# Optimization experiments

Measured on AMD Instinct MI355X. Metric: run time of the kernel, lower is better.

## Reference

```python
import jax, jax.numpy as jnp
import numpy as np

T, B, I, H, K = 200, 2048, 128, 128, 4


def setup_inputs() -> dict:
    key = jax.random.key(0)
    ks = jax.random.split(key, 7)
    inputs = jax.random.normal(ks[0], (T, B, I), jnp.float32)
    lengths = jax.random.randint(ks[1], (B,), 1, T + 1, jnp.int32)
    si = 1.0 / np.sqrt(I)
    sh = 1.0 / np.sqrt(H)
    w0 = jax.random.uniform(ks[2], (H,), jnp.float32, -sh, sh)      # Linear(H,1,bias=False)
    w1_w = jax.random.uniform(ks[3], (H, I), jnp.float32, -si, si)  # Linear(I,H)
    w1_b = jax.random.uniform(ks[4], (H,), jnp.float32, -si, si)
    w2_w = jax.random.uniform(ks[5], (H, I), jnp.float32, -si, si)  # Linear(I,H,bias=False)
    w3_w = jax.random.uniform(ks[6], (H, I), jnp.float32, -si, si)  # Linear(I,H,bias=False)
    return dict(inputs=inputs, lengths=lengths, label_len=4,
                w0=w0, w1_w=w1_w, w1_b=w1_b, w2_w=w2_w, w3_w=w3_w)


def reference(inputs, lengths, label_len, w0, w1_w, w1_b, w2_w, w3_w):
    # inputs: [T, B, I] time-major padded sequences; lengths: [B]
    T_, B_, _ = inputs.shape
    Kl = label_len
    dt = inputs.dtype
    # packed semantics: padded positions are exactly zero
    valid = (jnp.arange(T_)[:, None] < lengths[None, :])  # [T, B]
    x = inputs * valid[..., None].astype(dt)
    x1 = x @ w1_w.T + w1_b                                 # [T, B, H]
    x2 = x @ w2_w.T                                        # [T, B, H]
    # running mean m_s[t] = mean(inputs[:t+1]) (zeros at padding, as in torch)
    m_s = jnp.cumsum(x, axis=0) / jnp.arange(1, T_ + 1, dtype=dt)[:, None, None]
    # labeled timesteps: last min(L, label_len) steps of each sequence
    start = jnp.maximum(lengths - Kl, 0)                   # [B]
    t_lab = start[:, None] + jnp.arange(Kl)[None, :]       # [B, K]
    lab_valid = t_lab < lengths[:, None]                   # [B, K]
    t_c = jnp.minimum(t_lab, T_ - 1)
    b_idx = jnp.arange(B_)[:, None]
    x2_lab = x2[t_c, b_idx]                                # [B, K, H]
    wms_lab = m_s[t_c, b_idx] @ w3_w.T                     # [B, K, H]
    c = x2_lab + wms_lab                                   # [B, K, H]
    # att[b,k,s] = w0 . sigmoid(x1[s,b] + x2[t_k,b] + wms[t_k,b])
    att = jnp.einsum('sbkh,h->bks',
                     jax.nn.sigmoid(x1[:, :, None, :] + c[None, :, :, :]), w0)
    causal = (jnp.arange(T_)[None, None, :] <= t_lab[:, :, None]) & lab_valid[:, :, None]
    att = att * causal.astype(dt)                          # [B, K, T]
    h = jnp.einsum('bks,sbh->bkh', att, x1) + x2_lab       # [B, K, H]
    return h * lab_valid[..., None].astype(dt)
```

## Files before the change

kernel.cpp:

```cpp
#include <hip/hip_runtime.h>
#include <stdint.h>

#define T_DIM 200
#define B_DIM 2048
#define I_DIM 128
#define H_DIM 128
#define TS    32

typedef float  f32x4  __attribute__((ext_vector_type(4)));
typedef __bf16 bf16x8 __attribute__((ext_vector_type(8)));

union BF8 { ushort4 u2[2]; bf16x8 v; };

static __device__ __forceinline__ unsigned short f2bf(float f) {
    union { __bf16 b; unsigned short u; } c; c.b = (__bf16)f; return c.u;
}
static __device__ __forceinline__ float bf2f(unsigned short s) {
    union { unsigned u; float f; } c; c.u = ((unsigned)s) << 16;
    return c.f;
}
static __device__ __forceinline__ ushort4 cvt4(float4 v) {
    return make_ushort4(f2bf(v.x), f2bf(v.y), f2bf(v.z), f2bf(v.w));
}

__global__ __launch_bounds__(256, 4) void fused_kernel(
    const float* __restrict__ x, const int* __restrict__ lengths,
    const float* __restrict__ w0, const float* __restrict__ w1,
    const float* __restrict__ b1, const float* __restrict__ w2,
    const float* __restrict__ w3, float* __restrict__ out)
{
    __shared__ __align__(16) unsigned short xs[TS][136];
    __shared__ __align__(16) unsigned short x1s[TS][130];
    __shared__ __align__(16) float attp[TS][36];
    __shared__ __align__(16) float attk[TS][4];
    __shared__ __align__(16) float ektL[H_DIM][4];
    __shared__ __align__(16) float x2ls[4][H_DIM];
    __shared__ __align__(16) float w0s[H_DIM];
    __shared__ __align__(16) unsigned short axl[4][136];
    __shared__ __align__(16) unsigned short ams[4][136];

    const int b    = blockIdx.x;
    const int tid  = threadIdx.x;
    const int lane = tid & 63;
    const int wv   = tid >> 6;
    const int l15  = lane & 15;
    const int quad = lane >> 4;
    const int L     = lengths[b];
    const int start = (L > 4) ? (L - 4) : 0;
    const int nv    = (L < 4) ? L : 4;

    if (tid < 128) w0s[tid] = w0[tid];

    const int i = tid & 127;
    const float* xp = x + (size_t)b * I_DIM + i;
    float v0 = 0.f, v1 = 0.f, v2 = 0.f, v3 = 0.f;
    if (tid < 128) {
        v0 = xp[(size_t)(start + 0) * (B_DIM * I_DIM)];
        v1 = xp[(size_t)(start + 1) * (B_DIM * I_DIM)];
        v2 = xp[(size_t)(start + 2) * (B_DIM * I_DIM)];
        v3 = xp[(size_t)(start + 3) * (B_DIM * I_DIM)];
    }

    bf16x8 bfr[2][4];
    float  bias[2];
    #pragma unroll
    for (int nt = 0; nt < 2; ++nt) {
        const int n = wv * 32 + nt * 16 + l15;
        bias[nt] = b1[n];
        #pragma unroll
        for (int ks = 0; ks < 4; ++ks) {
            const int kc = ks * 32 + quad * 8;
            const float4 p0 = *(const float4*)(w1 + (size_t)n * I_DIM + kc);
            const float4 p1 = *(const float4*)(w1 + (size_t)n * I_DIM + kc + 4);
            BF8 t;
            t.u2[0] = cvt4(p0);
            t.u2[1] = cvt4(p1);
            bfr[nt][ks] = t.v;
        }
    }

    const int sr0 = tid >> 5;
    const int sf4 = tid & 31;
    {
        const float* xq = x + (size_t)b * I_DIM + sf4 * 4;
        const size_t RS = (size_t)B_DIM * I_DIM;
        f32x4 s0 = (f32x4){0.f, 0.f, 0.f, 0.f};
        f32x4 s1 = s0, s2 = s0, s3 = s0;
        int t = sr0;
        for (; t + 24 < start; t += 32) {
            s0 += *(const f32x4*)(xq + (size_t)(t     ) * RS);
            s1 += *(const f32x4*)(xq + (size_t)(t +  8) * RS);
            s2 += *(const f32x4*)(xq + (size_t)(t + 16) * RS);
            s3 += *(const f32x4*)(xq + (size_t)(t + 24) * RS);
        }
        for (; t < start; t += 8)
            s0 += *(const f32x4*)(xq + (size_t)t * RS);
        const f32x4 s = (s0 + s1) + (s2 + s3);
        float* psum = &attp[0][0];
        *(f32x4*)&psum[sr0 * 132 + sf4 * 4] = s;
    }
    __syncthreads();

    if (tid < 128) {
        const float* psum = &attp[0][0];
        float p = 0.f;
        #pragma unroll
        for (int g = 0; g < 8; ++g) p += psum[g * 132 + i];
        const float p0 = p + v0, p1 = p0 + v1, p2 = p1 + v2, p3 = p2 + v3;
        axl[0][i] = f2bf(v0); axl[1][i] = f2bf(v1);
        axl[2][i] = f2bf(v2); axl[3][i] = f2bf(v3);
        ams[0][i] = f2bf(p0 / (float)(start + 1));
        ams[1][i] = f2bf(p1 / (float)(start + 2));
        ams[2][i] = f2bf(p2 / (float)(start + 3));
        ams[3][i] = f2bf(p3 / (float)(start + 4));
    }
    __syncthreads();

    #pragma unroll
    for (int nt = 0; nt < 2; ++nt) {
        const int n = wv * 32 + nt * 16 + l15;
        f32x4 c1 = (f32x4){0.f, 0.f, 0.f, 0.f};
        f32x4 c2 = (f32x4){0.f, 0.f, 0.f, 0.f};
        #pragma unroll
        for (int ks = 0; ks < 4; ++ks) {
            const int kc = ks * 32 + quad * 8;
            const bf16x8 a1 = *(const bf16x8*)&axl[l15 & 3][kc];
            const bf16x8 a2 = *(const bf16x8*)&ams[l15 & 3][kc];
            const float4 q0 = *(const float4*)(w2 + (size_t)n * I_DIM + kc);
            const float4 q1 = *(const float4*)(w2 + (size_t)n * I_DIM + kc + 4);
            const float4 r0 = *(const float4*)(w3 + (size_t)n * I_DIM + kc);
            const float4 r1 = *(const float4*)(w3 + (size_t)n * I_DIM + kc + 4);
            BF8 bw2, bw3;
            bw2.u2[0] = cvt4(q0); bw2.u2[1] = cvt4(q1);
            bw3.u2[0] = cvt4(r0); bw3.u2[1] = cvt4(r1);
            c1 = __builtin_amdgcn_mfma_f32_16x16x32_bf16(a1, bw2.v, c1, 0, 0, 0);
            c2 = __builtin_amdgcn_mfma_f32_16x16x32_bf16(a2, bw3.v, c2, 0, 0, 0);
        }
        if (quad == 0) {
            #pragma unroll
            for (int r = 0; r < 4; ++r) {
                x2ls[r][n] = c1[r];
                ektL[n][r] = __builtin_amdgcn_exp2f(-1.44269504f * (c1[r] + c2[r]));
            }
        }
    }
    __syncthreads();

    const int sq = tid & 31;
    const int hg = tid >> 5;
    const int hcol = tid & 127;
    const int half = tid >> 7;
    float hacc0 = 0.f, hacc1 = 0.f, hacc2v = 0.f, hacc3 = 0.f;

    for (int t0 = 0; t0 < L; t0 += TS) {
        const int nrows = (L - t0 < TS) ? (L - t0) : TS;

        #pragma unroll
        for (int it = 0; it < 4; ++it) {
            const int sl = tid + it * 256;
            const int r = sl >> 5, f4 = sl & 31;
            ushort4 w = make_ushort4(0, 0, 0, 0);
            if (r < nrows) {
                const float4 v = *(const float4*)(
                    x + ((size_t)(t0 + r) * B_DIM + b) * I_DIM + f4 * 4);
                w = cvt4(v);
            }
            *(ushort4*)&xs[r][f4 * 4] = w;
        }
        __syncthreads();

        #pragma unroll
        for (int mt = 0; mt < 2; ++mt) {
            bf16x8 afr[4];
            #pragma unroll
            for (int ks = 0; ks < 4; ++ks)
                afr[ks] = *(const bf16x8*)&xs[mt * 16 + l15][ks * 32 + quad * 8];
            #pragma unroll
            for (int nt = 0; nt < 2; ++nt) {
                f32x4 acc = (f32x4){0.f, 0.f, 0.f, 0.f};
                #pragma unroll
                for (int ks = 0; ks < 4; ++ks)
                    acc = __builtin_amdgcn_mfma_f32_16x16x32_bf16(
                        afr[ks], bfr[nt][ks], acc, 0, 0, 0);
                const int h = wv * 32 + nt * 16 + l15;
                const int tr = mt * 16 + quad * 4;
                #pragma unroll
                for (int r = 0; r < 4; ++r)
                    x1s[tr + r][h] = f2bf(acc[r] + bias[nt]);
            }
        }
        __syncthreads();

        {
            const int h0 = hg * 16;
            f32x4 a = (f32x4){0.f, 0.f, 0.f, 0.f};
            #pragma unroll
            for (int hh = 0; hh < 16; hh += 2) {
                const int h = h0 + hh;
                const unsigned xv2 = *(const unsigned*)&x1s[sq][h];
                const float xa = bf2f((unsigned short)(xv2 & 0xFFFFu));
                const float xb = bf2f((unsigned short)(xv2 >> 16));
                const float Ea = __builtin_amdgcn_exp2f(-1.44269504f * xa);
                const float Eb = __builtin_amdgcn_exp2f(-1.44269504f * xb);
                const f32x4 eka = *(const f32x4*)&ektL[h][0];
                const f32x4 ekb = *(const f32x4*)&ektL[h + 1][0];
                const float wa = w0s[h], wb = w0s[h + 1];
                #pragma unroll
                for (int k = 0; k < 4; ++k)
                    a[k] += wa * __builtin_amdgcn_rcpf(1.f + Ea * eka[k])
                          + wb * __builtin_amdgcn_rcpf(1.f + Eb * ekb[k]);
            }
            #pragma unroll
            for (int k = 0; k < 4; ++k)
                a[k] += __shfl_xor(a[k], 32);
            if (!(tid & 32))
                *(f32x4*)&attp[sq][(tid >> 6) * 4] = a;
        }
        __syncthreads();

        if (tid < TS) {
            const int s = t0 + tid;
            f32x4 sm = (f32x4){0.f, 0.f, 0.f, 0.f};
            #pragma unroll
            for (int g = 0; g < 4; ++g)
                sm += *(const f32x4*)&attp[tid][g * 4];
            f32x4 o;
            o[0] = (0 < nv && s <= start    ) ? sm[0] : 0.f;
            o[1] = (1 < nv && s <= start + 1) ? sm[1] : 0.f;
            o[2] = (2 < nv && s <= start + 2) ? sm[2] : 0.f;
            o[3] = (3 < nv && s <= start + 3) ? sm[3] : 0.f;
            *(f32x4*)&attk[tid][0] = o;
        }
        __syncthreads();

        {
            const int sbase = half * 16;
            #pragma unroll
            for (int s2 = 0; s2 < 16; ++s2) {
                const int srow = sbase + s2;
                const f32x4 a4 = *(const f32x4*)&attk[srow][0];
                const float xv = bf2f(x1s[srow][hcol]);
                hacc0 += a4[0] * xv; hacc1 += a4[1] * xv;
                hacc2v += a4[2] * xv; hacc3 += a4[3] * xv;
            }
        }
        __syncthreads();
    }

    {
        float* h2 = &attp[0][0];
        if (half == 1) {
            *(f32x4*)&h2[hcol * 4] = (f32x4){hacc0, hacc1, hacc2v, hacc3};
        }
        __syncthreads();
        if (tid < 128) {
            const f32x4 o = *(const f32x4*)&h2[hcol * 4];
            hacc0 += o[0]; hacc1 += o[1]; hacc2v += o[2]; hacc3 += o[3];
            out[((size_t)b * 4 + 0) * H_DIM + hcol] = (0 < nv) ? hacc0 + x2ls[0][hcol] : 0.f;
            out[((size_t)b * 4 + 1) * H_DIM + hcol] = (1 < nv) ? hacc1 + x2ls[1][hcol] : 0.f;
            out[((size_t)b * 4 + 2) * H_DIM + hcol] = (2 < nv) ? hacc2v + x2ls[2][hcol] : 0.f;
            out[((size_t)b * 4 + 3) * H_DIM + hcol] = (3 < nv) ? hacc3 + x2ls[3][hcol] : 0.f;
        }
    }
}

extern "C" void kernel_launch(void* const* d_in, const int* in_sizes, int n_in,
                              void* d_out, int out_size, void* d_ws, size_t ws_size,
                              hipStream_t stream) {
    (void)in_sizes; (void)n_in; (void)out_size; (void)d_ws; (void)ws_size;
    const float* x       = (const float*)d_in[0];
    const int*   lengths = (const int*)d_in[1];
    const float* w0 = (const float*)d_in[3];
    const float* w1 = (const float*)d_in[4];
    const float* b1 = (const float*)d_in[5];
    const float* w2 = (const float*)d_in[6];
    const float* w3 = (const float*)d_in[7];
    float* out = (float*)d_out;

    fused_kernel<<<dim3(B_DIM), 256, 0, stream>>>(x, lengths, w0, w1, b1, w2, w3, out);
}
```

Baseline: 369.7 us.

## Use persistent blocks with atomic work queue and merge attention reduction stages

Launches a fixed grid of 1280 persistent blocks that pull batch indices from an atomic counter in the workspace. The aim is to balance the highly variable per-sequence lengths across CUs and to amortize the W1 fragment load. The attention row reduction now uses a per-wave 8-lane shuffle tree that writes masked results directly, which removes a shared-memory stage, one barrier and the trailing loop barrier. Occupancy hint rises to 5 blocks per SIMD. Costs are an extra memset launch and the serialization of the atomic fetch, and dropping the end-of-loop barrier risks a race between reads of x1s/attk and the next tile's writes.

```diff
diff --git a/kernel.cpp b/kernel.cpp
--- a/kernel.cpp
+++ b/kernel.cpp
@@ -23,11 +23,12 @@
     return make_ushort4(f2bf(v.x), f2bf(v.y), f2bf(v.z), f2bf(v.w));
 }
 
-__global__ __launch_bounds__(256, 4) void fused_kernel(
+__global__ __launch_bounds__(256, 5) void fused_kernel(
     const float* __restrict__ x, const int* __restrict__ lengths,
     const float* __restrict__ w0, const float* __restrict__ w1,
     const float* __restrict__ b1, const float* __restrict__ w2,
-    const float* __restrict__ w3, float* __restrict__ out)
+    const float* __restrict__ w3, float* __restrict__ out,
+    unsigned* __restrict__ wq)
 {
     __shared__ __align__(16) unsigned short xs[TS][136];
     __shared__ __align__(16) unsigned short x1s[TS][130];
@@ -38,28 +39,15 @@
     __shared__ __align__(16) float w0s[H_DIM];
     __shared__ __align__(16) unsigned short axl[4][136];
     __shared__ __align__(16) unsigned short ams[4][136];
-
-    const int b    = blockIdx.x;
+    __shared__ int b_sh;
+
     const int tid  = threadIdx.x;
     const int lane = tid & 63;
     const int wv   = tid >> 6;
     const int l15  = lane & 15;
     const int quad = lane >> 4;
-    const int L     = lengths[b];
-    const int start = (L > 4) ? (L - 4) : 0;
-    const int nv    = (L < 4) ? L : 4;
 
     if (tid < 128) w0s[tid] = w0[tid];
-
-    const int i = tid & 127;
-    const float* xp = x + (size_t)b * I_DIM + i;
-    float v0 = 0.f, v1 = 0.f, v2 = 0.f, v3 = 0.f;
-    if (tid < 128) {
-        v0 = xp[(size_t)(start + 0) * (B_DIM * I_DIM)];
-        v1 = xp[(size_t)(start + 1) * (B_DIM * I_DIM)];
-        v2 = xp[(size_t)(start + 2) * (B_DIM * I_DIM)];
-        v3 = xp[(size_t)(start + 3) * (B_DIM * I_DIM)];
-    }
 
     bf16x8 bfr[2][4];
     float  bias[2];
@@ -81,185 +69,207 @@
 
     const int sr0 = tid >> 5;
     const int sf4 = tid & 31;
-    {
-        const float* xq = x + (size_t)b * I_DIM + sf4 * 4;
-        const size_t RS = (size_t)B_DIM * I_DIM;
-        f32x4 s0 = (f32x4){0.f, 0.f, 0.f, 0.f};
-        f32x4 s1 = s0, s2 = s0, s3 = s0;
-        int t = sr0;
-        for (; t + 24 < start; t += 32) {
-            s0 += *(const f32x4*)(xq + (size_t)(t     ) * RS);
-            s1 += *(const f32x4*)(xq + (size_t)(t +  8) * RS);
-            s2 += *(const f32x4*)(xq + (size_t)(t + 16) * RS);
-            s3 += *(const f32x4*)(xq + (size_t)(t + 24) * RS);
-        }
-        for (; t < start; t += 8)
-            s0 += *(const f32x4*)(xq + (size_t)t * RS);
-        const f32x4 s = (s0 + s1) + (s2 + s3);
-        float* psum = &attp[0][0];
-        *(f32x4*)&psum[sr0 * 132 + sf4 * 4] = s;
-    }
-    __syncthreads();
-
-    if (tid < 128) {
-        const float* psum = &attp[0][0];
-        float p = 0.f;
-        #pragma unroll
-        for (int g = 0; g < 8; ++g) p += psum[g * 132 + i];
-        const float p0 = p + v0, p1 = p0 + v1, p2 = p1 + v2, p3 = p2 + v3;
-        axl[0][i] = f2bf(v0); axl[1][i] = f2bf(v1);
-        axl[2][i] = f2bf(v2); axl[3][i] = f2bf(v3);
-        ams[0][i] = f2bf(p0 / (float)(start + 1));
-        ams[1][i] = f2bf(p1 / (float)(start + 2));
-        ams[2][i] = f2bf(p2 / (float)(start + 3));
-        ams[3][i] = f2bf(p3 / (float)(start + 4));
-    }
-    __syncthreads();
-
-    #pragma unroll
-    for (int nt = 0; nt < 2; ++nt) {
-        const int n = wv * 32 + nt * 16 + l15;
-        f32x4 c1 = (f32x4){0.f, 0.f, 0.f, 0.f};
-        f32x4 c2 = (f32x4){0.f, 0.f, 0.f, 0.f};
-        #pragma unroll
-        for (int ks = 0; ks < 4; ++ks) {
-            const int kc = ks * 32 + quad * 8;
-            const bf16x8 a1 = *(const bf16x8*)&axl[l15 & 3][kc];
-            const bf16x8 a2 = *(const bf16x8*)&ams[l15 & 3][kc];
-            const float4 q0 = *(const float4*)(w2 + (size_t)n * I_DIM + kc);
-            const float4 q1 = *(const float4*)(w2 + (size_t)n * I_DIM + kc + 4);
-            const float4 r0 = *(const float4*)(w3 + (size_t)n * I_DIM + kc);
-            const float4 r1 = *(const float4*)(w3 + (size_t)n * I_DIM + kc + 4);
-            BF8 bw2, bw3;
-            bw2.u2[0] = cvt4(q0); bw2.u2[1] = cvt4(q1);
-            bw3.u2[0] = cvt4(r0); bw3.u2[1] = cvt4(r1);
-            c1 = __builtin_amdgcn_mfma_f32_16x16x32_bf16(a1, bw2.v, c1, 0, 0, 0);
-            c2 = __builtin_amdgcn_mfma_f32_16x16x32_bf16(a2, bw3.v, c2, 0, 0, 0);
-        }
-        if (quad == 0) {
-            #pragma unroll
-            for (int r = 0; r < 4; ++r) {
-                x2ls[r][n] = c1[r];
-                ektL[n][r] = __builtin_amdgcn_exp2f(-1.44269504f * (c1[r] + c2[r]));
-            }
-        }
-    }
-    __syncthreads();
-
-    const int sq = tid & 31;
-    const int hg = tid >> 5;
+    const int i   = tid & 127;
     const int hcol = tid & 127;
     const int half = tid >> 7;
-    float hacc0 = 0.f, hacc1 = 0.f, hacc2v = 0.f, hacc3 = 0.f;
-
-    for (int t0 = 0; t0 < L; t0 += TS) {
-        const int nrows = (L - t0 < TS) ? (L - t0) : TS;
+    const int rE  = wv * 8 + (lane >> 3);
+    const int hE0 = (lane & 7) * 16;
+
+    int bprev = -1;
+    for (;;) {
+        int b;
+        if (wq) {
+            if (tid == 0) b_sh = (int)atomicAdd(wq, 1u);
+            __syncthreads();
+            b = b_sh;
+        } else {
+            if (bprev >= 0) break;
+            b = blockIdx.x;
+        }
+        if (b >= B_DIM) break;
+        bprev = b;
+
+        const int L     = lengths[b];
+        const int start = (L > 4) ? (L - 4) : 0;
+        const int nv    = (L < 4) ? L : 4;
+
+        const float* xp = x + (size_t)b * I_DIM + i;
+        float v0 = 0.f, v1 = 0.f, v2 = 0.f, v3 = 0.f;
+        if (tid < 128) {
+            v0 = xp[(size_t)(start + 0) * (B_DIM * I_DIM)];
+            v1 = xp[(size_t)(start + 1) * (B_DIM * I_DIM)];
+            v2 = xp[(size_t)(start + 2) * (B_DIM * I_DIM)];
+            v3 = xp[(size_t)(start + 3) * (B_DIM * I_DIM)];
+        }
+
+        {
+            const float* xq = x + (size_t)b * I_DIM + sf4 * 4;
+            const size_t RS = (size_t)B_DIM * I_DIM;
+            f32x4 s0 = (f32x4){0.f, 0.f, 0.f, 0.f};
+            f32x4 s1 = s0, s2 = s0, s3 = s0;
+            int t = sr0;
+            for (; t + 24 < start; t += 32) {
+                s0 += *(const f32x4*)(xq + (size_t)(t     ) * RS);
+                s1 += *(const f32x4*)(xq + (size_t)(t +  8) * RS);
+                s2 += *(const f32x4*)(xq + (size_t)(t + 16) * RS);
+                s3 += *(const f32x4*)(xq + (size_t)(t + 24) * RS);
+            }
+            for (; t < start; t += 8)
+                s0 += *(const f32x4*)(xq + (size_t)t * RS);
+            const f32x4 s = (s0 + s1) + (s2 + s3);
+            float* psum = &attp[0][0];
+            *(f32x4*)&psum[sr0 * 132 + sf4 * 4] = s;
+        }
+        __syncthreads();
+
+        if (tid < 128) {
+            const float* psum = &attp[0][0];
+            float p = 0.f;
+            #pragma unroll
+            for (int g = 0; g < 8; ++g) p += psum[g * 132 + i];
+            const float p0 = p + v0, p1 = p0 + v1, p2 = p1 + v2, p3 = p2 + v3;
+            axl[0][i] = f2bf(v0); axl[1][i] = f2bf(v1);
+            axl[2][i] = f2bf(v2); axl[3][i] = f2bf(v3);
+            ams[0][i] = f2bf(p0 / (float)(start + 1));
+            ams[1][i] = f2bf(p1 / (float)(start + 2));
+            ams[2][i] = f2bf(p2 / (float)(start + 3));
+            ams[3][i] = f2bf(p3 / (float)(start + 4));
+        }
+        __syncthreads();
 
         #pragma unroll
-        for (int it = 0; it < 4; ++it) {
-            const int sl = tid + it * 256;
-            const int r = sl >> 5, f4 = sl & 31;
-            ushort4 w = make_ushort4(0, 0, 0, 0);
-            if (r < nrows) {
-                const float4 v = *(const float4*)(
-                    x + ((size_t)(t0 + r) * B_DIM + b) * I_DIM + f4 * 4);
-                w = cvt4(v);
-            }
-            *(ushort4*)&xs[r][f4 * 4] = w;
+        for (int nt = 0; nt < 2; ++nt) {
+            const int n = wv * 32 + nt * 16 + l15;
+            f32x4 c1 = (f32x4){0.f, 0.f, 0.f, 0.f};
+            f32x4 c2 = (f32x4){0.f, 0.f, 0.f, 0.f};
+            #pragma unroll
+            for (int ks = 0; ks < 4; ++ks) {
+                const int kc = ks * 32 + quad * 8;
+                const bf16x8 a1 = *(const bf16x8*)&axl[l15 & 3][kc];
+                const bf16x8 a2 = *(const bf16x8*)&ams[l15 & 3][kc];
+                const float4 q0 = *(const float4*)(w2 + (size_t)n * I_DIM + kc);
+                const float4 q1 = *(const float4*)(w2 + (size_t)n * I_DIM + kc + 4);
+                const float4 r0 = *(const float4*)(w3 + (size_t)n * I_DIM + kc);
+                const float4 r1 = *(const float4*)(w3 + (size_t)n * I_DIM + kc + 4);
+                BF8 bw2, bw3;
+                bw2.u2[0] = cvt4(q0); bw2.u2[1] = cvt4(q1);
+                bw3.u2[0] = cvt4(r0); bw3.u2[1] = cvt4(r1);
+                c1 = __builtin_amdgcn_mfma_f32_16x16x32_bf16(a1, bw2.v, c1, 0, 0, 0);
+                c2 = __builtin_amdgcn_mfma_f32_16x16x32_bf16(a2, bw3.v, c2, 0, 0, 0);
+            }
+            if (quad == 0) {
+                #pragma unroll
+                for (int r = 0; r < 4; ++r) {
+                    x2ls[r][n] = c1[r];
+                    ektL[n][r] = __builtin_amdgcn_exp2f(-1.44269504f * (c1[r] + c2[r]));
+                }
+            }
         }
         __syncthreads();
 
-        #pragma unroll
-        for (int mt = 0; mt < 2; ++mt) {
-            bf16x8 afr[4];
+        float hacc0 = 0.f, hacc1 = 0.f, hacc2v = 0.f, hacc3 = 0.f;
+
+        for (int t0 = 0; t0 < L; t0 += TS) {
+            const int nrows = (L - t0 < TS) ? (L - t0) : TS;
+
             #pragma unroll
-            for (int ks = 0; ks < 4; ++ks)
-                afr[ks] = *(const bf16x8*)&xs[mt * 16 + l15][ks * 32 + quad * 8];
+            for (int it = 0; it < 4; ++it) {
+                const int sl = tid + it * 256;
+                const int r = sl >> 5, f4 = sl & 31;
+                ushort4 w = make_ushort4(0, 0, 0, 0);
+                if (r < nrows) {
+                    const float4 v = *(const float4*)(
+                        x + ((size_t)(t0 + r) * B_DIM + b) * I_DIM + f4 * 4);
+                    w = cvt4(v);
+                }
+                *(ushort4*)&xs[r][f4 * 4] = w;
+            }
+            __syncthreads();
+
             #pragma unroll
-            for (int nt = 0; nt < 2; ++nt) {
-                f32x4 acc = (f32x4){0.f, 0.f, 0.f, 0.f};
+            for (int mt = 0; mt < 2; ++mt) {
+                bf16x8 afr[4];
                 #pragma unroll
                 for (int ks = 0; ks < 4; ++ks)
-                    acc = __builtin_amdgcn_mfma_f32_16x16x32_bf16(
-                        afr[ks], bfr[nt][ks], acc, 0, 0, 0);
-                const int h = wv * 32 + nt * 16 + l15;
-                const int tr = mt * 16 + quad * 4;
-                #pragma unroll
-                for (int r = 0; r < 4; ++r)
-                    x1s[tr + r][h] = f2bf(acc[r] + bias[nt]);
-            }
-        }
-        __syncthreads();
+                    afr[ks] = *(const bf16x8*)&xs[mt * 16 + l15][ks * 32 + quad * 8];
+                #pragma unroll
+                for (int nt = 0; nt < 2; ++nt) {
+                    f32x4 acc = (f32x4){0.f, 0.f, 0.f, 0.f};
+                    #pragma unroll
+                    for (int ks = 0; ks < 4; ++ks)
+                        acc = __builtin_amdgcn_mfma_f32_16x16x32_bf16(
+                            afr[ks], bfr[nt][ks], acc, 0, 0, 0);
+                    const int h = wv * 32 + nt * 16 + l15;
+                    const int tr = mt * 16 + quad * 4;
+                    #pragma unroll
+                    for (int r = 0; r < 4; ++r)
+                        x1s[tr + r][h] = f2bf(acc[r] + bias[nt]);
+                }
+            }
+            __syncthreads();
+
+            {
+                f32x4 a = (f32x4){0.f, 0.f, 0.f, 0.f};
+                #pragma unroll
+                for (int hh = 0; hh < 16; hh += 2) {
+                    const int h = hE0 + hh;
+                    const unsigned xv2 = *(const unsigned*)&x1s[rE][h];
+                    const float xa = bf2f((unsigned short)(xv2 & 0xFFFFu));
+                    const float xb = bf2f((unsigned short)(xv2 >> 16));
+                    const float Ea = __builtin_amdgcn_exp2f(-1.44269504f * xa);
+                    const float Eb = __builtin_amdgcn_exp2f(-1.44269504f * xb);
+                    const f32x4 eka = *(const f32x4*)&ektL[h][0];
+                    const f32x4 ekb = *(const f32x4*)&ektL[h + 1][0];
+                    const float wa = w0s[h], wb = w0s[h + 1];
+                    #pragma unroll
+                    for (int k = 0; k < 4; ++k)
+                        a[k] += wa * __builtin_amdgcn_rcpf(1.f + Ea * eka[k])
+                              + wb * __builtin_amdgcn_rcpf(1.f + Eb * ekb[k]);
+                }
+                #pragma unroll
+                for (int m = 1; m <= 4; m <<= 1)
+                    #pragma unroll
+                    for (int k = 0; k < 4; ++k)
+                        a[k] += __shfl_xor(a[k], m);
+                if ((lane & 7) == 0) {
+                    const int s = t0 + rE;
+                    f32x4 o;
+                    o[0] = (0 < nv && s <= start    ) ? a[0] : 0.f;
+                    o[1] = (1 < nv && s <= start + 1) ? a[1] : 0.f;
+                    o[2] = (2 < nv && s <= start + 2) ? a[2] : 0.f;
+                    o[3] = (3 < nv && s <= start + 3) ? a[3] : 0.f;
+                    *(f32x4*)&attk[rE][0] = o;
+                }
+            }
+            __syncthreads();
+
+            {
+                const int sbase = half * 16;
+                #pragma unroll
+                for (int s2 = 0; s2 < 16; ++s2) {
+                    const int srow = sbase + s2;
+                    const f32x4 a4 = *(const f32x4*)&attk[srow][0];
+                    const float xv = bf2f(x1s[srow][hcol]);
+                    hacc0 += a4[0] * xv; hacc1 += a4[1] * xv;
+                    hacc2v += a4[2] * xv; hacc3 += a4[3] * xv;
+                }
+            }
+        }
 
         {
-            const int h0 = hg * 16;
-            f32x4 a = (f32x4){0.f, 0.f, 0.f, 0.f};
-            #pragma unroll
-            for (int hh = 0; hh < 16; hh += 2) {
-                const int h = h0 + hh;
-                const unsigned xv2 = *(const unsigned*)&x1s[sq][h];
-                const float xa = bf2f((unsigned short)(xv2 & 0xFFFFu));
-                const float xb = bf2f((unsigned short)(xv2 >> 16));
-                const float Ea = __builtin_amdgcn_exp2f(-1.44269504f * xa);
-                const float Eb = __builtin_amdgcn_exp2f(-1.44269504f * xb);
-                const f32x4 eka = *(const f32x4*)&ektL[h][0];
-                const f32x4 ekb = *(const f32x4*)&ektL[h + 1][0];
-                const float wa = w0s[h], wb = w0s[h + 1];
-                #pragma unroll
-                for (int k = 0; k < 4; ++k)
-                    a[k] += wa * __builtin_amdgcn_rcpf(1.f + Ea * eka[k])
-                          + wb * __builtin_amdgcn_rcpf(1.f + Eb * ekb[k]);
-            }
-            #pragma unroll
-            for (int k = 0; k < 4; ++k)
-                a[k] += __shfl_xor(a[k], 32);
-            if (!(tid & 32))
-                *(f32x4*)&attp[sq][(tid >> 6) * 4] = a;
-        }
-        __syncthreads();
-
-        if (tid < TS) {
-            const int s = t0 + tid;
-            f32x4 sm = (f32x4){0.f, 0.f, 0.f, 0.f};
-            #pragma unroll
-            for (int g = 0; g < 4; ++g)
-                sm += *(const f32x4*)&attp[tid][g * 4];
-            f32x4 o;
-            o[0] = (0 < nv && s <= start    ) ? sm[0] : 0.f;
-            o[1] = (1 < nv && s <= start + 1) ? sm[1] : 0.f;
-            o[2] = (2 < nv && s <= start + 2) ? sm[2] : 0.f;
-            o[3] = (3 < nv && s <= start + 3) ? sm[3] : 0.f;
-            *(f32x4*)&attk[tid][0] = o;
-        }
-        __syncthreads();
-
-        {
-            const int sbase = half * 16;
-            #pragma unroll
-            for (int s2 = 0; s2 < 16; ++s2) {
-                const int srow = sbase + s2;
-                const f32x4 a4 = *(const f32x4*)&attk[srow][0];
-                const float xv = bf2f(x1s[srow][hcol]);
-                hacc0 += a4[0] * xv; hacc1 += a4[1] * xv;
-                hacc2v += a4[2] * xv; hacc3 += a4[3] * xv;
-            }
-        }
-        __syncthreads();
-    }
-
-    {
-        float* h2 = &attp[0][0];
-        if (half == 1) {
-            *(f32x4*)&h2[hcol * 4] = (f32x4){hacc0, hacc1, hacc2v, hacc3};
-        }
-        __syncthreads();
-        if (tid < 128) {
-            const f32x4 o = *(const f32x4*)&h2[hcol * 4];
-            hacc0 += o[0]; hacc1 += o[1]; hacc2v += o[2]; hacc3 += o[3];
-            out[((size_t)b * 4 + 0) * H_DIM + hcol] = (0 < nv) ? hacc0 + x2ls[0][hcol] : 0.f;
-            out[((size_t)b * 4 + 1) * H_DIM + hcol] = (1 < nv) ? hacc1 + x2ls[1][hcol] : 0.f;
-            out[((size_t)b * 4 + 2) * H_DIM + hcol] = (2 < nv) ? hacc2v + x2ls[2][hcol] : 0.f;
-            out[((size_t)b * 4 + 3) * H_DIM + hcol] = (3 < nv) ? hacc3 + x2ls[3][hcol] : 0.f;
+            float* h2 = &attp[0][0];
+            if (half == 1) {
+                *(f32x4*)&h2[hcol * 4] = (f32x4){hacc0, hacc1, hacc2v, hacc3};
+            }
+            __syncthreads();
+            if (tid < 128) {
+                const f32x4 o = *(const f32x4*)&h2[hcol * 4];
+                hacc0 += o[0]; hacc1 += o[1]; hacc2v += o[2]; hacc3 += o[3];
+                out[((size_t)b * 4 + 0) * H_DIM + hcol] = (0 < nv) ? hacc0 + x2ls[0][hcol] : 0.f;
+                out[((size_t)b * 4 + 1) * H_DIM + hcol] = (1 < nv) ? hacc1 + x2ls[1][hcol] : 0.f;
+                out[((size_t)b * 4 + 2) * H_DIM + hcol] = (2 < nv) ? hacc2v + x2ls[2][hcol] : 0.f;
+                out[((size_t)b * 4 + 3) * H_DIM + hcol] = (3 < nv) ? hacc3 + x2ls[3][hcol] : 0.f;
+            }
         }
     }
 }
@@ -267,7 +277,7 @@
 extern "C" void kernel_launch(void* const* d_in, const int* in_sizes, int n_in,
                               void* d_out, int out_size, void* d_ws, size_t ws_size,
                               hipStream_t stream) {
-    (void)in_sizes; (void)n_in; (void)out_size; (void)d_ws; (void)ws_size;
+    (void)in_sizes; (void)n_in; (void)out_size;
     const float* x       = (const float*)d_in[0];
     const int*   lengths = (const int*)d_in[1];
     const float* w0 = (const float*)d_in[3];
@@ -277,5 +287,14 @@
     const float* w3 = (const float*)d_in[7];
     float* out = (float*)d_out;
 
-    fused_kernel<<<dim3(B_DIM), 256, 0, stream>>>(x, lengths, w0, w1, b1, w2, w3, out);
-}
+    unsigned* wq = (d_ws != nullptr && ws_size >= sizeof(unsigned))
+                       ? (unsigned*)d_ws : nullptr;
+    if (wq) {
+        hipMemsetAsync(wq, 0, sizeof(unsigned), stream);
+        fused_kernel<<<dim3(1280), 256, 0, stream>>>(
+            x, lengths, w0, w1, b1, w2, w3, out, wq);
+    } else {
+        fused_kernel<<<dim3(B_DIM), 256, 0, stream>>>(
+            x, lengths, w0, w1, b1, w2, w3, out, nullptr);
+    }
+}
```

New measurement: 420.5 us. +13.7%, slower.
